# Kernel tuning notes

Measured on AMD Instinct MI355X. Metric: run time of the kernel, lower is better.

Reference implementation:

```python
import jax, jax.numpy as jnp
import numpy as np

B, H, S, D = 4, 16, 2048, 64
SCALE = float(D ** 0.5)


def setup_inputs() -> dict:
    key = jax.random.key(0)
    kq, kk, kv = jax.random.split(key, 3)
    q = jax.random.normal(kq, (B, H, S, D), dtype=jnp.float32)
    k = jax.random.normal(kk, (B, H, S, D), dtype=jnp.float32)
    v = jax.random.normal(kv, (B, H, S, D), dtype=jnp.float32)
    return {"q": q, "k": k, "v": v}


def reference(q, k, v):
    # score: (B, H, S, S)
    score = jnp.einsum('bhqd,bhkd->bhqk', q, k) / SCALE
    seq_len = q.shape[-2]
    # causal mask: True above the diagonal (future positions) -> -inf
    mask = jnp.triu(jnp.ones((seq_len, seq_len), dtype=bool), k=1)
    score = jnp.where(mask, -jnp.inf, score)
    attn = jax.nn.softmax(score, axis=-1)
    return jnp.einsum('bhqk,bhkd->bhqd', attn, v)
```

## Files before the change

### kernel.cpp

```cpp
#include <hip/hip_runtime.h>
#include <math.h>

constexpr int S = 2048, D = 64;
constexpr int BH = 64;
constexpr int QTILE = 256;
constexpr int KVB = 64;
constexpr float QSCALE = 0.18033688011112042f;
constexpr float MBIAS = -8.0f;

typedef float f32x4 __attribute__((ext_vector_type(4)));
typedef float f32x16 __attribute__((ext_vector_type(16)));
typedef _Float16 f16x8 __attribute__((ext_vector_type(8)));
typedef unsigned int u32;
typedef unsigned int u32x2 __attribute__((ext_vector_type(2)));
typedef unsigned int u32x4 __attribute__((ext_vector_type(4)));

#define MFMA32(a, b, c) __builtin_amdgcn_mfma_f32_32x32x16_f16((a), (b), (c), 0, 0, 0)

#if __has_builtin(__builtin_amdgcn_exp2f)
#define EXP2(x) __builtin_amdgcn_exp2f(x)
#else
#define EXP2(x) exp2f(x)
#endif

__device__ __forceinline__ u32 pkbits(float a, float b) {
  return __builtin_bit_cast(u32, __builtin_amdgcn_cvt_pkrtz(a, b));
}
__device__ __forceinline__ void plswap(u32& a, u32& b) {
  asm volatile("v_permlane32_swap_b32 %0, %1" : "+v"(a), "+v"(b));
}
__device__ __forceinline__ int swzb(int row) { return ((row & 7) ^ (row >> 3)) << 3; }

#define BARRIER_LGKM()                                          \
  do {                                                          \
    asm volatile("s_waitcnt lgkmcnt(0)" ::: "memory");          \
    __builtin_amdgcn_s_barrier();                               \
    __builtin_amdgcn_sched_barrier(0);                          \
  } while (0)

__device__ __forceinline__ void compute_tile(
    const int kt, const int Rp, const int q32, const int hi,
    const _Float16* __restrict__ Kb, const _Float16* __restrict__ Vb,
    const f16x8 (&bq)[4], f32x16& od0, f32x16& od1, float& l) {
  const int ck = kt * KVB;
  if (ck > Rp + 31) return;
  const int rel = Rp - ck;
  const int ctmax = (rel >= 32) ? 1 : 0;
  const bool needmask = (32 * ctmax + 31 > rel);

  f32x16 st0, st1;
#pragma unroll
  for (int r = 0; r < 16; ++r) { st0[r] = MBIAS; st1[r] = MBIAS; }
  __builtin_amdgcn_s_setprio(1);
#pragma unroll
  for (int t = 0; t < 4; ++t) {
    f16x8 a = *(const f16x8*)&Kb[(q32 << 6) + (swzb(q32) ^ (16 * t + 8 * hi))];
    st0 = MFMA32(a, bq[t], st0);
  }
  if (ctmax) {
    const int row = 32 + q32;
#pragma unroll
    for (int t = 0; t < 4; ++t) {
      f16x8 a = *(const f16x8*)&Kb[(row << 6) + (swzb(row) ^ (16 * t + 8 * hi))];
      st1 = MFMA32(a, bq[t], st1);
    }
  }
  __builtin_amdgcn_s_setprio(0);

  if (needmask) {
    const int qrel = rel + q32;
#pragma unroll
    for (int gq = 0; gq < 4; ++gq)
#pragma unroll
      for (int i = 0; i < 4; ++i) {
        if (8 * gq + 4 * hi + i > qrel) st0[4 * gq + i] = -INFINITY;
        if (ctmax && (32 + 8 * gq + 4 * hi + i > qrel)) st1[4 * gq + i] = -INFINITY;
      }
  }

  float ps = 0.f;
#pragma unroll
  for (int r = 0; r < 16; ++r) { const float p = EXP2(st0[r]); st0[r] = p; ps += p; }
  if (ctmax)
#pragma unroll
    for (int r = 0; r < 16; ++r) { const float p = EXP2(st1[r]); st1[r] = p; ps += p; }
  l += ps;

  __builtin_amdgcn_s_setprio(1);
#define PV_CT(stv, CT)                                                          \
  _Pragma("unroll")                                                             \
  for (int t = 0; t < 2; ++t) {                                                 \
    u32 x0 = pkbits(stv[8 * t + 0], stv[8 * t + 1]);                            \
    u32 x1 = pkbits(stv[8 * t + 2], stv[8 * t + 3]);                            \
    u32 y0 = pkbits(stv[8 * t + 4], stv[8 * t + 5]);                            \
    u32 y1 = pkbits(stv[8 * t + 6], stv[8 * t + 7]);                            \
    plswap(x0, y0); plswap(x1, y1);                                             \
    const f16x8 pf = __builtin_bit_cast(f16x8, (u32x4){x0, x1, y0, y1});        \
    const int kcol = (2 * (CT) + t) * 16 + 8 * hi;                              \
    { const f16x8 vf = *(const f16x8*)&Vb[(q32 << 6) + (swzb(q32) ^ kcol)];     \
      od0 = MFMA32(vf, pf, od0); }                                              \
    { const int row = 32 + q32;                                                 \
      const f16x8 vf = *(const f16x8*)&Vb[(row << 6) + (swzb(row) ^ kcol)];     \
      od1 = MFMA32(vf, pf, od1); }                                              \
  }
  PV_CT(st0, 0);
  if (ctmax) { PV_CT(st1, 1); }
#undef PV_CT
  __builtin_amdgcn_s_setprio(0);
}

__global__ __launch_bounds__(512, 2)
void attn_fwd(const float* __restrict__ qp, const float* __restrict__ kp,
              const float* __restrict__ vp, float* __restrict__ op) {
  __shared__ _Float16 Kl[4][KVB * 64];
  __shared__ _Float16 Vt[4][64 * KVB];

  const int bh = blockIdx.x;
  const int pa = blockIdx.y;

  const int tid = threadIdx.x;
  const int wid = tid >> 6;
  const int lane = tid & 63;
  const int q32 = lane & 31;
  const int hi = lane >> 5;

  const size_t base = (size_t)bh * (S * D);

  const int rp = tid >> 4;
  const int cg = tid & 15;
  const int r0 = 2 * rp, r1 = 2 * rp + 1;
  const int c4 = cg * 4;
  const int kw0 = (r0 << 6) + (swzb(r0) ^ c4);
  const int kw1 = (r1 << 6) + (swzb(r1) ^ c4);
  const int vw0 = ((c4 + 0) << 6) + (swzb(c4 + 0) ^ r0);
  const int vw1 = ((c4 + 1) << 6) + (swzb(c4 + 1) ^ r0);
  const int vw2 = ((c4 + 2) << 6) + (swzb(c4 + 2) ^ r0);
  const int vw3 = ((c4 + 3) << 6) + (swzb(c4 + 3) ^ r0);

  const float* kbase = kp + base + (size_t)r0 * D + c4;
  const float* vbase = vp + base + (size_t)r0 * D + c4;

#define LOADT(kt, K0, K1, V0, V1)                                        \
  do {                                                                   \
    const float* kg_ = kbase + ((size_t)(kt) << 12);                     \
    const float* vg_ = vbase + ((size_t)(kt) << 12);                     \
    K0 = *(const f32x4*)kg_; K1 = *(const f32x4*)(kg_ + D);              \
    V0 = *(const f32x4*)vg_; V1 = *(const f32x4*)(vg_ + D);              \
  } while (0)

#define WRITET(buf, K0, K1, V0, V1)                                      \
  do {                                                                   \
    u32x2 kA_, kB_;                                                      \
    kA_[0] = pkbits(K0[0], K0[1]); kA_[1] = pkbits(K0[2], K0[3]);        \
    kB_[0] = pkbits(K1[0], K1[1]); kB_[1] = pkbits(K1[2], K1[3]);        \
    *(u32x2*)&Kl[buf][kw0] = kA_;                                        \
    *(u32x2*)&Kl[buf][kw1] = kB_;                                        \
    *(u32*)&Vt[buf][vw0] = pkbits(V0[0], V1[0]);                         \
    *(u32*)&Vt[buf][vw1] = pkbits(V0[1], V1[1]);                         \
    *(u32*)&Vt[buf][vw2] = pkbits(V0[2], V1[2]);                         \
    *(u32*)&Vt[buf][vw3] = pkbits(V0[3], V1[3]);                         \
  } while (0)

  f32x4 ka0, ka1, va0, va1, kb0, kb1, vb0, vb1;

  for (int ph = 0; ph < 2; ++ph) {
    const int qt = ph ? (7 - pa) : pa;
    const int Rp = qt * QTILE + wid * 32;
    const int NT = 4 * qt + 4;

    f16x8 bq[4];
    {
      const float* qg = qp + base + (size_t)(Rp + q32) * D + 8 * hi;
#pragma unroll
      for (int t = 0; t < 4; ++t) {
        f32x4 a = *(const f32x4*)(qg + 16 * t);
        f32x4 b = *(const f32x4*)(qg + 16 * t + 4);
#pragma unroll
        for (int j = 0; j < 4; ++j) bq[t][j] = (_Float16)(a[j] * QSCALE);
#pragma unroll
        for (int j = 0; j < 4; ++j) bq[t][4 + j] = (_Float16)(b[j] * QSCALE);
      }
    }

    f32x16 od0 = {}, od1 = {};
    float l = 0.f;

    LOADT(0, ka0, ka1, va0, va1);
    LOADT(1, kb0, kb1, vb0, vb1);

    for (int ktp = 0; ktp < NT; ktp += 2) {
      const int b0 = ktp & 2;
      WRITET(b0, ka0, ka1, va0, va1);
      WRITET(b0 + 1, kb0, kb1, vb0, vb1);
      if (ktp + 2 < NT) {
        LOADT(ktp + 2, ka0, ka1, va0, va1);
        LOADT(ktp + 3, kb0, kb1, vb0, vb1);
      }
      BARRIER_LGKM();
      compute_tile(ktp, Rp, q32, hi, Kl[b0], Vt[b0], bq, od0, od1, l);
      compute_tile(ktp + 1, Rp, q32, hi, Kl[b0 + 1], Vt[b0 + 1], bq, od0, od1, l);
    }

    const float lt = l + __shfl_xor(l, 32);
    const float inv = 1.f / lt;
    float* og = op + base + (size_t)(Rp + q32) * D + 4 * hi;
#pragma unroll
    for (int gq = 0; gq < 4; ++gq) {
      f32x4 w0, w1;
#pragma unroll
      for (int i = 0; i < 4; ++i) w0[i] = od0[4 * gq + i] * inv;
#pragma unroll
      for (int i = 0; i < 4; ++i) w1[i] = od1[4 * gq + i] * inv;
      *(f32x4*)(og + 8 * gq) = w0;
      *(f32x4*)(og + 32 + 8 * gq) = w1;
    }
  }
#undef LOADT
#undef WRITET
}

extern "C" void kernel_launch(void* const* d_in, const int* in_sizes, int n_in,
                              void* d_out, int out_size, void* d_ws, size_t ws_size,
                              hipStream_t stream) {
  const float* q = (const float*)d_in[0];
  const float* k = (const float*)d_in[1];
  const float* v = (const float*)d_in[2];
  float* out = (float*)d_out;
  dim3 grid(BH, 4);
  attn_fwd<<<grid, 512, 0, stream>>>(q, k, v, out);
}
```

Before: 58.85 us.

## Double-buffer four KV tiles per barrier with register prefetch across compute

The KV staging is restructured into groups of four 64-row tiles held in two LDS buffer sets. The global loads for the next group are issued before the current group's compute, and the converted fp16 data is written to the other buffer set afterwards, so only one barrier is needed per four tiles. K staging also changes so each thread loads 8 contiguous floats and writes one 16-byte LDS store. This doubles LDS use to 128 KB, which drops residency to one block per CU, and adds 64 VGPRs of staging registers, which risks spills under the 512x2 launch bound.

```diff
diff --git a/kernel.cpp b/kernel.cpp
--- a/kernel.cpp
+++ b/kernel.cpp
@@ -12,7 +12,6 @@
 typedef float f32x16 __attribute__((ext_vector_type(16)));
 typedef _Float16 f16x8 __attribute__((ext_vector_type(8)));
 typedef unsigned int u32;
-typedef unsigned int u32x2 __attribute__((ext_vector_type(2)));
 typedef unsigned int u32x4 __attribute__((ext_vector_type(4)));
 
 #define MFMA32(a, b, c) __builtin_amdgcn_mfma_f32_32x32x16_f16((a), (b), (c), 0, 0, 0)
@@ -112,8 +111,8 @@
 __global__ __launch_bounds__(512, 2)
 void attn_fwd(const float* __restrict__ qp, const float* __restrict__ kp,
               const float* __restrict__ vp, float* __restrict__ op) {
-  __shared__ _Float16 Kl[4][KVB * 64];
-  __shared__ _Float16 Vt[4][64 * KVB];
+  __shared__ _Float16 Kl[8][KVB * 64];
+  __shared__ _Float16 Vt[8][64 * KVB];
 
   const int bh = blockIdx.x;
   const int pa = blockIdx.y;
@@ -126,47 +125,46 @@
 
   const size_t base = (size_t)bh * (S * D);
 
-  const int rp = tid >> 4;
-  const int cg = tid & 15;
-  const int r0 = 2 * rp, r1 = 2 * rp + 1;
-  const int c4 = cg * 4;
-  const int kw0 = (r0 << 6) + (swzb(r0) ^ c4);
-  const int kw1 = (r1 << 6) + (swzb(r1) ^ c4);
-  const int vw0 = ((c4 + 0) << 6) + (swzb(c4 + 0) ^ r0);
-  const int vw1 = ((c4 + 1) << 6) + (swzb(c4 + 1) ^ r0);
-  const int vw2 = ((c4 + 2) << 6) + (swzb(c4 + 2) ^ r0);
-  const int vw3 = ((c4 + 3) << 6) + (swzb(c4 + 3) ^ r0);
-
-  const float* kbase = kp + base + (size_t)r0 * D + c4;
-  const float* vbase = vp + base + (size_t)r0 * D + c4;
+  const int rowK = tid >> 3;
+  const int c8 = (tid & 7) << 3;
+  const int kw = (rowK << 6) + (swzb(rowK) ^ c8);
+  const float* kbase = kp + base + (size_t)rowK * D + c8;
+
+  const int rpv = tid >> 4;
+  const int c4 = (tid & 15) << 2;
+  const int rv0 = 2 * rpv;
+  const int vw0 = ((c4 + 0) << 6) + (swzb(c4 + 0) ^ rv0);
+  const int vw1 = ((c4 + 1) << 6) + (swzb(c4 + 1) ^ rv0);
+  const int vw2 = ((c4 + 2) << 6) + (swzb(c4 + 2) ^ rv0);
+  const int vw3 = ((c4 + 3) << 6) + (swzb(c4 + 3) ^ rv0);
+  const float* vbase = vp + base + (size_t)rv0 * D + c4;
 
 #define LOADT(kt, K0, K1, V0, V1)                                        \
   do {                                                                   \
     const float* kg_ = kbase + ((size_t)(kt) << 12);                     \
     const float* vg_ = vbase + ((size_t)(kt) << 12);                     \
-    K0 = *(const f32x4*)kg_; K1 = *(const f32x4*)(kg_ + D);              \
+    K0 = *(const f32x4*)kg_; K1 = *(const f32x4*)(kg_ + 4);              \
     V0 = *(const f32x4*)vg_; V1 = *(const f32x4*)(vg_ + D);              \
   } while (0)
 
 #define WRITET(buf, K0, K1, V0, V1)                                      \
   do {                                                                   \
-    u32x2 kA_, kB_;                                                      \
-    kA_[0] = pkbits(K0[0], K0[1]); kA_[1] = pkbits(K0[2], K0[3]);        \
-    kB_[0] = pkbits(K1[0], K1[1]); kB_[1] = pkbits(K1[2], K1[3]);        \
-    *(u32x2*)&Kl[buf][kw0] = kA_;                                        \
-    *(u32x2*)&Kl[buf][kw1] = kB_;                                        \
+    u32x4 kq_;                                                           \
+    kq_[0] = pkbits(K0[0], K0[1]); kq_[1] = pkbits(K0[2], K0[3]);        \
+    kq_[2] = pkbits(K1[0], K1[1]); kq_[3] = pkbits(K1[2], K1[3]);        \
+    *(u32x4*)&Kl[buf][kw] = kq_;                                         \
     *(u32*)&Vt[buf][vw0] = pkbits(V0[0], V1[0]);                         \
     *(u32*)&Vt[buf][vw1] = pkbits(V0[1], V1[1]);                         \
     *(u32*)&Vt[buf][vw2] = pkbits(V0[2], V1[2]);                         \
     *(u32*)&Vt[buf][vw3] = pkbits(V0[3], V1[3]);                         \
   } while (0)
 
-  f32x4 ka0, ka1, va0, va1, kb0, kb1, vb0, vb1;
+  f32x4 sk0[4], sk1[4], sv0[4], sv1[4];
 
   for (int ph = 0; ph < 2; ++ph) {
     const int qt = ph ? (7 - pa) : pa;
     const int Rp = qt * QTILE + wid * 32;
-    const int NT = 4 * qt + 4;
+    const int NG = qt + 1;
 
     f16x8 bq[4];
     {
@@ -185,20 +183,32 @@
     f32x16 od0 = {}, od1 = {};
     float l = 0.f;
 
-    LOADT(0, ka0, ka1, va0, va1);
-    LOADT(1, kb0, kb1, vb0, vb1);
-
-    for (int ktp = 0; ktp < NT; ktp += 2) {
-      const int b0 = ktp & 2;
-      WRITET(b0, ka0, ka1, va0, va1);
-      WRITET(b0 + 1, kb0, kb1, vb0, vb1);
-      if (ktp + 2 < NT) {
-        LOADT(ktp + 2, ka0, ka1, va0, va1);
-        LOADT(ktp + 3, kb0, kb1, vb0, vb1);
+#pragma unroll
+    for (int i = 0; i < 4; ++i) LOADT(i, sk0[i], sk1[i], sv0[i], sv1[i]);
+    BARRIER_LGKM();
+#pragma unroll
+    for (int i = 0; i < 4; ++i) WRITET(i, sk0[i], sk1[i], sv0[i], sv1[i]);
+    BARRIER_LGKM();
+
+    for (int g = 0; g < NG; ++g) {
+      const int bb = (g & 1) << 2;
+      const bool more = (g + 1 < NG);
+      if (more) {
+#pragma unroll
+        for (int i = 0; i < 4; ++i)
+          LOADT(4 * (g + 1) + i, sk0[i], sk1[i], sv0[i], sv1[i]);
+      }
+#pragma unroll
+      for (int i = 0; i < 4; ++i)
+        compute_tile(4 * g + i, Rp, q32, hi, Kl[bb + i], Vt[bb + i],
+                     bq, od0, od1, l);
+      if (more) {
+        const int nb = bb ^ 4;
+#pragma unroll
+        for (int i = 0; i < 4; ++i)
+          WRITET(nb + i, sk0[i], sk1[i], sv0[i], sv1[i]);
       }
       BARRIER_LGKM();
-      compute_tile(ktp, Rp, q32, hi, Kl[b0], Vt[b0], bq, od0, od1, l);
-      compute_tile(ktp + 1, Rp, q32, hi, Kl[b0 + 1], Vt[b0 + 1], bq, od0, od1, l);
     }
 
     const float lt = l + __shfl_xor(l, 32);
```

New measurement: 78.61 us. +33.6%, slower.

## Split each KV tile across two wave groups with LDS reduction of partial outputs

Applied to the files above, without the earlier changes.

Doubles the block to 1024 threads, so each query group of 32 rows is handled by two waves, each covering one 32-key half of every 64-key tile. Partial outputs and row sums are combined through shared memory at the end of each query tile. Each half-wave also loads and writes only one of the two staged KV tiles. This raises per-CU wave parallelism and shortens per-wave dependency chains, at the cost of an extra LDS reduction, more barriers, and a larger shared-memory footprint that may limit how many blocks fit per CU.

```diff
diff --git a/kernel.cpp b/kernel.cpp
--- a/kernel.cpp
+++ b/kernel.cpp
@@ -38,96 +38,90 @@
     __builtin_amdgcn_sched_barrier(0);                          \
   } while (0)
 
-__device__ __forceinline__ void compute_tile(
-    const int kt, const int Rp, const int q32, const int hi,
+__device__ __forceinline__ void compute_half(
+    const int kt, const int kh, const int Rp, const int q32, const int hi,
     const _Float16* __restrict__ Kb, const _Float16* __restrict__ Vb,
     const f16x8 (&bq)[4], f32x16& od0, f32x16& od1, float& l) {
-  const int ck = kt * KVB;
+  const int ck = kt * KVB + 32 * kh;
   if (ck > Rp + 31) return;
   const int rel = Rp - ck;
-  const int ctmax = (rel >= 32) ? 1 : 0;
-  const bool needmask = (32 * ctmax + 31 > rel);
-
-  f32x16 st0, st1;
-#pragma unroll
-  for (int r = 0; r < 16; ++r) { st0[r] = MBIAS; st1[r] = MBIAS; }
+  const bool needmask = (rel == 0);
+
+  f32x16 st;
+#pragma unroll
+  for (int r = 0; r < 16; ++r) st[r] = MBIAS;
+  const int krow = 32 * kh + q32;
+  const int swk = swzb(krow);
   __builtin_amdgcn_s_setprio(1);
 #pragma unroll
   for (int t = 0; t < 4; ++t) {
-    f16x8 a = *(const f16x8*)&Kb[(q32 << 6) + (swzb(q32) ^ (16 * t + 8 * hi))];
-    st0 = MFMA32(a, bq[t], st0);
-  }
-  if (ctmax) {
-    const int row = 32 + q32;
-#pragma unroll
-    for (int t = 0; t < 4; ++t) {
-      f16x8 a = *(const f16x8*)&Kb[(row << 6) + (swzb(row) ^ (16 * t + 8 * hi))];
-      st1 = MFMA32(a, bq[t], st1);
-    }
+    f16x8 a = *(const f16x8*)&Kb[(krow << 6) + (swk ^ (16 * t + 8 * hi))];
+    st = MFMA32(a, bq[t], st);
   }
   __builtin_amdgcn_s_setprio(0);
 
   if (needmask) {
-    const int qrel = rel + q32;
 #pragma unroll
     for (int gq = 0; gq < 4; ++gq)
 #pragma unroll
-      for (int i = 0; i < 4; ++i) {
-        if (8 * gq + 4 * hi + i > qrel) st0[4 * gq + i] = -INFINITY;
-        if (ctmax && (32 + 8 * gq + 4 * hi + i > qrel)) st1[4 * gq + i] = -INFINITY;
-      }
-  }
-
-  float ps = 0.f;
-#pragma unroll
-  for (int r = 0; r < 16; ++r) { const float p = EXP2(st0[r]); st0[r] = p; ps += p; }
-  if (ctmax)
-#pragma unroll
-    for (int r = 0; r < 16; ++r) { const float p = EXP2(st1[r]); st1[r] = p; ps += p; }
-  l += ps;
+      for (int i = 0; i < 4; ++i)
+        if (8 * gq + 4 * hi + i > q32) st[4 * gq + i] = -INFINITY;
+  }
+
+  float p0 = 0.f, p1 = 0.f, p2 = 0.f, p3 = 0.f;
+#pragma unroll
+  for (int r = 0; r < 4; ++r) {
+    float a = EXP2(st[4 * r + 0]); st[4 * r + 0] = a; p0 += a;
+    float b = EXP2(st[4 * r + 1]); st[4 * r + 1] = b; p1 += b;
+    float c = EXP2(st[4 * r + 2]); st[4 * r + 2] = c; p2 += c;
+    float d = EXP2(st[4 * r + 3]); st[4 * r + 3] = d; p3 += d;
+  }
+  l += (p0 + p1) + (p2 + p3);
 
   __builtin_amdgcn_s_setprio(1);
-#define PV_CT(stv, CT)                                                          \
-  _Pragma("unroll")                                                             \
-  for (int t = 0; t < 2; ++t) {                                                 \
-    u32 x0 = pkbits(stv[8 * t + 0], stv[8 * t + 1]);                            \
-    u32 x1 = pkbits(stv[8 * t + 2], stv[8 * t + 3]);                            \
-    u32 y0 = pkbits(stv[8 * t + 4], stv[8 * t + 5]);                            \
-    u32 y1 = pkbits(stv[8 * t + 6], stv[8 * t + 7]);                            \
-    plswap(x0, y0); plswap(x1, y1);                                             \
-    const f16x8 pf = __builtin_bit_cast(f16x8, (u32x4){x0, x1, y0, y1});        \
-    const int kcol = (2 * (CT) + t) * 16 + 8 * hi;                              \
-    { const f16x8 vf = *(const f16x8*)&Vb[(q32 << 6) + (swzb(q32) ^ kcol)];     \
-      od0 = MFMA32(vf, pf, od0); }                                              \
-    { const int row = 32 + q32;                                                 \
-      const f16x8 vf = *(const f16x8*)&Vb[(row << 6) + (swzb(row) ^ kcol)];     \
-      od1 = MFMA32(vf, pf, od1); }                                              \
-  }
-  PV_CT(st0, 0);
-  if (ctmax) { PV_CT(st1, 1); }
-#undef PV_CT
+  const int rowv1 = 32 + q32;
+  const int sw0 = swzb(q32), sw1 = swzb(rowv1);
+#pragma unroll
+  for (int t = 0; t < 2; ++t) {
+    u32 x0 = pkbits(st[8 * t + 0], st[8 * t + 1]);
+    u32 x1 = pkbits(st[8 * t + 2], st[8 * t + 3]);
+    u32 y0 = pkbits(st[8 * t + 4], st[8 * t + 5]);
+    u32 y1 = pkbits(st[8 * t + 6], st[8 * t + 7]);
+    plswap(x0, y0); plswap(x1, y1);
+    const f16x8 pf = __builtin_bit_cast(f16x8, (u32x4){x0, x1, y0, y1});
+    const int kcol = 32 * kh + t * 16 + 8 * hi;
+    const f16x8 vf0 = *(const f16x8*)&Vb[(q32 << 6) + (sw0 ^ kcol)];
+    const f16x8 vf1 = *(const f16x8*)&Vb[(rowv1 << 6) + (sw1 ^ kcol)];
+    od0 = MFMA32(vf0, pf, od0);
+    od1 = MFMA32(vf1, pf, od1);
+  }
   __builtin_amdgcn_s_setprio(0);
 }
 
-__global__ __launch_bounds__(512, 2)
+__global__ __launch_bounds__(1024, 4)
 void attn_fwd(const float* __restrict__ qp, const float* __restrict__ kp,
               const float* __restrict__ vp, float* __restrict__ op) {
-  __shared__ _Float16 Kl[4][KVB * 64];
-  __shared__ _Float16 Vt[4][64 * KVB];
+  __shared__ __align__(16) unsigned char smem[69632];
+  _Float16* Kl = (_Float16*)smem;
+  _Float16* Vt = (_Float16*)(smem + 32768);
+  float* red = (float*)smem;
 
   const int bh = blockIdx.x;
   const int pa = blockIdx.y;
 
   const int tid = threadIdx.x;
-  const int wid = tid >> 6;
   const int lane = tid & 63;
   const int q32 = lane & 31;
   const int hi = lane >> 5;
+  const int wid = tid >> 6;
+  const int qg = wid & 7;
+  const int kh = wid >> 3;
 
   const size_t base = (size_t)bh * (S * D);
 
-  const int rp = tid >> 4;
-  const int cg = tid & 15;
+  const int stid = tid & 511;
+  const int rp = stid >> 4;
+  const int cg = stid & 15;
   const int r0 = 2 * rp, r1 = 2 * rp + 1;
   const int c4 = cg * 4;
   const int kw0 = (r0 << 6) + (swzb(r0) ^ c4);
@@ -136,45 +130,46 @@
   const int vw1 = ((c4 + 1) << 6) + (swzb(c4 + 1) ^ r0);
   const int vw2 = ((c4 + 2) << 6) + (swzb(c4 + 2) ^ r0);
   const int vw3 = ((c4 + 3) << 6) + (swzb(c4 + 3) ^ r0);
-
   const float* kbase = kp + base + (size_t)r0 * D + c4;
   const float* vbase = vp + base + (size_t)r0 * D + c4;
 
-#define LOADT(kt, K0, K1, V0, V1)                                        \
+#define LOADT(kt)                                                        \
   do {                                                                   \
     const float* kg_ = kbase + ((size_t)(kt) << 12);                     \
     const float* vg_ = vbase + ((size_t)(kt) << 12);                     \
-    K0 = *(const f32x4*)kg_; K1 = *(const f32x4*)(kg_ + D);              \
-    V0 = *(const f32x4*)vg_; V1 = *(const f32x4*)(vg_ + D);              \
+    sk0 = *(const f32x4*)kg_; sk1 = *(const f32x4*)(kg_ + D);            \
+    sv0 = *(const f32x4*)vg_; sv1 = *(const f32x4*)(vg_ + D);            \
   } while (0)
 
-#define WRITET(buf, K0, K1, V0, V1)                                      \
+#define WRITET(buf)                                                      \
   do {                                                                   \
     u32x2 kA_, kB_;                                                      \
-    kA_[0] = pkbits(K0[0], K0[1]); kA_[1] = pkbits(K0[2], K0[3]);        \
-    kB_[0] = pkbits(K1[0], K1[1]); kB_[1] = pkbits(K1[2], K1[3]);        \
-    *(u32x2*)&Kl[buf][kw0] = kA_;                                        \
-    *(u32x2*)&Kl[buf][kw1] = kB_;                                        \
-    *(u32*)&Vt[buf][vw0] = pkbits(V0[0], V1[0]);                         \
-    *(u32*)&Vt[buf][vw1] = pkbits(V0[1], V1[1]);                         \
-    *(u32*)&Vt[buf][vw2] = pkbits(V0[2], V1[2]);                         \
-    *(u32*)&Vt[buf][vw3] = pkbits(V0[3], V1[3]);                         \
+    kA_[0] = pkbits(sk0[0], sk0[1]); kA_[1] = pkbits(sk0[2], sk0[3]);    \
+    kB_[0] = pkbits(sk1[0], sk1[1]); kB_[1] = pkbits(sk1[2], sk1[3]);    \
+    _Float16* kb_ = Kl + ((buf) << 12);                                  \
+    _Float16* vb_ = Vt + ((buf) << 12);                                  \
+    *(u32x2*)&kb_[kw0] = kA_;                                            \
+    *(u32x2*)&kb_[kw1] = kB_;                                            \
+    *(u32*)&vb_[vw0] = pkbits(sv0[0], sv1[0]);                           \
+    *(u32*)&vb_[vw1] = pkbits(sv0[1], sv1[1]);                           \
+    *(u32*)&vb_[vw2] = pkbits(sv0[2], sv1[2]);                           \
+    *(u32*)&vb_[vw3] = pkbits(sv0[3], sv1[3]);                           \
   } while (0)
 
-  f32x4 ka0, ka1, va0, va1, kb0, kb1, vb0, vb1;
+  f32x4 sk0, sk1, sv0, sv1;
 
   for (int ph = 0; ph < 2; ++ph) {
     const int qt = ph ? (7 - pa) : pa;
-    const int Rp = qt * QTILE + wid * 32;
+    const int Rp = qt * QTILE + qg * 32;
     const int NT = 4 * qt + 4;
 
     f16x8 bq[4];
     {
-      const float* qg = qp + base + (size_t)(Rp + q32) * D + 8 * hi;
+      const float* qg_ = qp + base + (size_t)(Rp + q32) * D + 8 * hi;
 #pragma unroll
       for (int t = 0; t < 4; ++t) {
-        f32x4 a = *(const f32x4*)(qg + 16 * t);
-        f32x4 b = *(const f32x4*)(qg + 16 * t + 4);
+        f32x4 a = *(const f32x4*)(qg_ + 16 * t);
+        f32x4 b = *(const f32x4*)(qg_ + 16 * t + 4);
 #pragma unroll
         for (int j = 0; j < 4; ++j) bq[t][j] = (_Float16)(a[j] * QSCALE);
 #pragma unroll
@@ -185,35 +180,51 @@
     f32x16 od0 = {}, od1 = {};
     float l = 0.f;
 
-    LOADT(0, ka0, ka1, va0, va1);
-    LOADT(1, kb0, kb1, vb0, vb1);
+    LOADT(kh);
 
     for (int ktp = 0; ktp < NT; ktp += 2) {
       const int b0 = ktp & 2;
-      WRITET(b0, ka0, ka1, va0, va1);
-      WRITET(b0 + 1, kb0, kb1, vb0, vb1);
-      if (ktp + 2 < NT) {
-        LOADT(ktp + 2, ka0, ka1, va0, va1);
-        LOADT(ktp + 3, kb0, kb1, vb0, vb1);
+      WRITET(b0 + kh);
+      if (ktp + 2 < NT) LOADT(ktp + 2 + kh);
+      BARRIER_LGKM();
+      compute_half(ktp, kh, Rp, q32, hi, Kl + (b0 << 12), Vt + (b0 << 12),
+                   bq, od0, od1, l);
+      compute_half(ktp + 1, kh, Rp, q32, hi, Kl + ((b0 + 1) << 12),
+                   Vt + ((b0 + 1) << 12), bq, od0, od1, l);
+    }
+
+    BARRIER_LGKM();
+    if (kh == 1) {
+      float* rw = red + qg * (33 * 64);
+#pragma unroll
+      for (int r = 0; r < 16; ++r) rw[r * 64 + lane] = od0[r];
+#pragma unroll
+      for (int r = 0; r < 16; ++r) rw[(16 + r) * 64 + lane] = od1[r];
+      rw[32 * 64 + lane] = l;
+    }
+    BARRIER_LGKM();
+    if (kh == 0) {
+      const float* rr = red + qg * (33 * 64);
+#pragma unroll
+      for (int r = 0; r < 16; ++r) od0[r] += rr[r * 64 + lane];
+#pragma unroll
+      for (int r = 0; r < 16; ++r) od1[r] += rr[(16 + r) * 64 + lane];
+      l += rr[32 * 64 + lane];
+      const float lt = l + __shfl_xor(l, 32);
+      const float inv = 1.f / lt;
+      float* og = op + base + (size_t)(Rp + q32) * D + 4 * hi;
+#pragma unroll
+      for (int gq2 = 0; gq2 < 4; ++gq2) {
+        f32x4 w0, w1;
+#pragma unroll
+        for (int i = 0; i < 4; ++i) w0[i] = od0[4 * gq2 + i] * inv;
+#pragma unroll
+        for (int i = 0; i < 4; ++i) w1[i] = od1[4 * gq2 + i] * inv;
+        *(f32x4*)(og + 8 * gq2) = w0;
+        *(f32x4*)(og + 32 + 8 * gq2) = w1;
       }
-      BARRIER_LGKM();
-      compute_tile(ktp, Rp, q32, hi, Kl[b0], Vt[b0], bq, od0, od1, l);
-      compute_tile(ktp + 1, Rp, q32, hi, Kl[b0 + 1], Vt[b0 + 1], bq, od0, od1, l);
-    }
-
-    const float lt = l + __shfl_xor(l, 32);
-    const float inv = 1.f / lt;
-    float* og = op + base + (size_t)(Rp + q32) * D + 4 * hi;
-#pragma unroll
-    for (int gq = 0; gq < 4; ++gq) {
-      f32x4 w0, w1;
-#pragma unroll
-      for (int i = 0; i < 4; ++i) w0[i] = od0[4 * gq + i] * inv;
-#pragma unroll
-      for (int i = 0; i < 4; ++i) w1[i] = od1[4 * gq + i] * inv;
-      *(f32x4*)(og + 8 * gq) = w0;
-      *(f32x4*)(og + 32 + 8 * gq) = w1;
-    }
+    }
+    BARRIER_LGKM();
   }
 #undef LOADT
 #undef WRITET
@@ -227,5 +238,5 @@
   const float* v = (const float*)d_in[2];
   float* out = (float*)d_out;
   dim3 grid(BH, 4);
-  attn_fwd<<<grid, 512, 0, stream>>>(q, k, v, out);
-}
+  attn_fwd<<<grid, 1024, 0, stream>>>(q, k, v, out);
+}
```

New measurement: 133.5 us. 2.27x slower.
